# Kernel optimization log

Hardware: AMD Instinct MI355X
Metric: run time of the kernel (lower is better)

## Reference

```python
import jax, jax.numpy as jnp
import numpy as np

N = 16384      # number of nodes (pos rows)
S = 16384      # number of src nodes (src_pos rows)
E = 262144     # number of edges (COO entries)
D = 512        # embed_dim
H = 8          # num_heads
HD = D // H    # head_dim = 64
HID = 1024     # mlp hidden
MLP_IN = D + 3 * H  # 536
EPS = 1e-5


def layer_norm(x, g, b):
    mu = jnp.mean(x, axis=-1, keepdims=True)
    var = jnp.mean((x - mu) ** 2, axis=-1, keepdims=True)
    return (x - mu) * jax.lax.rsqrt(var + EPS) * g + b


def setup_inputs() -> dict:
    key = jax.random.key(0)
    ks = jax.random.split(key, 20)
    s = 1.0 / np.sqrt(D)
    sh = 1.0 / np.sqrt(HID)
    return {
        "x": jax.random.normal(ks[0], (N, D), jnp.float32),
        "Wq": jax.random.uniform(ks[1], (D, D), jnp.float32, -s, s),
        "bq": jnp.zeros((D,), jnp.float32),
        "Wk": jax.random.uniform(ks[2], (D, D), jnp.float32, -s, s),
        "bk": jnp.zeros((D,), jnp.float32),
        "g_att": jnp.ones((D,), jnp.float32),
        "b_att": jnp.zeros((D,), jnp.float32),
        "g_mlp": jnp.ones((D,), jnp.float32),
        "b_mlp": jnp.zeros((D,), jnp.float32),
        "W_in": jax.random.uniform(ks[3], (HID, MLP_IN), jnp.float32, -s, s),
        "b_in": jnp.zeros((HID,), jnp.float32),
        "W_out": jax.random.uniform(ks[4], (D, HID), jnp.float32, -sh, sh),
        "b_out": jnp.zeros((D,), jnp.float32),
        "att_bias": jax.random.normal(ks[5], (H, E), jnp.float32),
        "dist": jax.random.uniform(ks[6], (E,), jnp.float32, 0.5, 6.0),
        "pos": jax.random.normal(ks[7], (N, 3), jnp.float32),
        "src_pos": jax.random.normal(ks[8], (S, 3), jnp.float32),
        "row_index": jax.random.randint(ks[9], (E,), 0, N),
        "src_index": jax.random.randint(ks[10], (E,), 0, S),
        "org_to_src": jax.random.randint(ks[11], (S,), 0, N),
    }


def reference(x, Wq, bq, Wk, bk, g_att, b_att, g_mlp, b_mlp, W_in, b_in,
              W_out, b_out, att_bias, dist, pos, src_pos,
              row_index, src_index, org_to_src):
    n = x.shape[0]
    z = layer_norm(x, g_att, b_att)
    q = (z @ Wq.T + bq).reshape(n, H, HD)          # [N,H,hd]
    k = (z @ Wk.T + bk).reshape(n, H, HD)          # [N,H,hd]
    k_src = k[org_to_src]                          # [S,H,hd]
    # per-edge masked logits: q[row] . k_src[col] / sqrt(hd) + bias
    qe = q[row_index]                              # [E,H,hd]
    ke = k_src[src_index]                          # [E,H,hd]
    logits = jnp.einsum('ehd,ehd->eh', qe, ke) / jnp.sqrt(jnp.float32(HD))
    logits = logits + att_bias.T                   # [E,H]
    # segment (per-row) softmax over incident edges
    m = jax.ops.segment_max(logits, row_index, num_segments=n)
    p = jnp.exp(logits - m[row_index])
    den = jax.ops.segment_sum(p, row_index, num_segments=n)
    att = p / den[row_index]                       # [E,H]
    inv = jnp.where(dist == 0, 0.0, 1.0 / dist)[:, None]
    att = att * inv
    # sparse bmm: feat[h,row] += att * src_pos[col]; rowsum for centering
    sp = src_pos[src_index]                        # [E,3]
    feat = jax.ops.segment_sum(att[:, :, None] * sp[:, None, :],
                               row_index, num_segments=n)   # [N,H,3]
    rowsum = jax.ops.segment_sum(att, row_index, num_segments=n)  # [N,H]
    feat = feat - rowsum[:, :, None] * pos[:, None, :]
    feat = feat.reshape(n, H * 3)
    z2 = layer_norm(x, g_mlp, b_mlp)
    h = jax.nn.gelu(jnp.concatenate([z2, feat], axis=-1) @ W_in.T + b_in)
    return x + (h @ W_out.T + b_out)
```

## Files before the change

### kernel.cpp

```cpp
#include <hip/hip_runtime.h>
#include <math.h>


typedef unsigned short u16;
typedef __attribute__((ext_vector_type(8))) short bf16x8;
typedef __attribute__((ext_vector_type(4))) float f32x4;
typedef __attribute__((ext_vector_type(2))) float f32x2;

constexpr int N_NODES = 16384;
constexpr int E_EDGES = 262144;
constexpr int D = 512;
constexpr int KIN = 576;

constexpr size_t OFF_ZATT = 0;
constexpr size_t OFF_ZCAT = 16777216;
constexpr size_t OFF_WQK  = 35651584;
constexpr size_t OFF_BQK  = 36700160;
constexpr size_t OFF_WIN  = 36704256;
constexpr size_t OFF_WOUT = 37883904;
constexpr size_t OFF_QK   = 38932480;
constexpr size_t OFF_CNT  = 55709696;
constexpr size_t OFF_BKT  = 55775232;
constexpr size_t OFF_HBF  = 59969536;

static __device__ __forceinline__ u16 f2bf(float f) {
  union { float f; unsigned int u; } v; v.f = f;
  unsigned int u = v.u;
  u = u + 0x7FFFu + ((u >> 16) & 1u);
  return (u16)(u >> 16);
}
static __device__ __forceinline__ void gload16(const u16* g, u16* l) {
  __builtin_amdgcn_global_load_lds(
      (const __attribute__((address_space(1))) unsigned int*)g,
      (__attribute__((address_space(3))) unsigned int*)l, 16, 0, 0);
}

__global__ __launch_bounds__(256) void prep_weights(
    const float* __restrict__ Wq, const float* __restrict__ Wk,
    const float* __restrict__ bq, const float* __restrict__ bk,
    const float* __restrict__ W_in, const float* __restrict__ W_out,
    const int* __restrict__ row_index,
    u16* __restrict__ wqk, float* __restrict__ bqk,
    u16* __restrict__ win, u16* __restrict__ wout,
    int* __restrict__ cnt, int* __restrict__ bucket)
{
  const int gid = blockIdx.x * 256 + threadIdx.x;
  if (gid < 512 * 1024) {
    wqk[gid]  = f2bf(gid < 512 * 512 ? Wq[gid] : Wk[gid - 512 * 512]);
    wout[gid] = f2bf(W_out[gid]);
  }
  if (gid < 1024 * KIN) {
    const int r = gid / KIN, c = gid - r * KIN;
    win[gid] = f2bf(c < 536 ? W_in[r * 536 + c] : 0.f);
  }
  if (gid < 1024) bqk[gid] = gid < 512 ? bq[gid] : bk[gid - 512];
  if (gid < E_EDGES) {
    const int r = row_index[gid];
    const int p = atomicAdd(&cnt[r], 1);
    if (p < 64) bucket[(size_t)r * 64 + p] = gid;
  }
}

__global__ __launch_bounds__(256) void ln_kernel(
    const float* __restrict__ x,
    const float* __restrict__ g1, const float* __restrict__ b1,
    const float* __restrict__ g2, const float* __restrict__ b2,
    u16* __restrict__ zatt, u16* __restrict__ zcat)
{
  const int row = blockIdx.x;
  const int t = threadIdx.x;
  const float2 v = *(const float2*)(x + (size_t)row * D + t * 2);
  float s = v.x + v.y;
  float s2 = v.x * v.x + v.y * v.y;
#pragma unroll
  for (int m = 1; m < 64; m <<= 1) {
    s  += __shfl_xor(s, m, 64);
    s2 += __shfl_xor(s2, m, 64);
  }
  __shared__ float red[8];
  const int wv = t >> 6;
  if ((t & 63) == 0) { red[wv] = s; red[4 + wv] = s2; }
  __syncthreads();
  s  = red[0] + red[1] + red[2] + red[3];
  s2 = red[4] + red[5] + red[6] + red[7];
  const float mu = s * (1.f / D);
  const float var = s2 * (1.f / D) - mu * mu;
  const float rs = rsqrtf(var + 1e-5f);
  const int c0 = t * 2;
  const float n0 = (v.x - mu) * rs, n1 = (v.y - mu) * rs;
  zatt[(size_t)row * D + c0]       = f2bf(n0 * g1[c0] + b1[c0]);
  zatt[(size_t)row * D + c0 + 1]   = f2bf(n1 * g1[c0 + 1] + b1[c0 + 1]);
  zcat[(size_t)row * KIN + c0]     = f2bf(n0 * g2[c0] + b2[c0]);
  zcat[(size_t)row * KIN + c0 + 1] = f2bf(n1 * g2[c0 + 1] + b2[c0 + 1]);
  if (t < 64) zcat[(size_t)row * KIN + D + t] = 0;
}

template <int EPI, int WPE>
__global__ __launch_bounds__(256, WPE) void gemm_nt(
    const u16* __restrict__ A, const u16* __restrict__ B,
    const float* __restrict__ bias, const float* __restrict__ resid,
    void* __restrict__ Cout, int M, int Nn, int K)
{
  constexpr int BM = 128, BN = 128, BK = 32;
  __shared__ __align__(16) u16 As[2 * BM * BK];
  __shared__ __align__(16) u16 Bs[2 * BN * BK];
  const int tid = threadIdx.x;
  const int lane = tid & 63;
  const int wave = tid >> 6;
  const int m0 = blockIdx.x * BM;
  const int n0 = blockIdx.y * BN;
  const int wm = (wave >> 1) * 64;
  const int wn = (wave & 1) * 64;
  const int fr = lane & 15;
  const int fq = lane >> 4;
  const int srow = lane >> 2;
  const int skoff = (lane & 3) * 8;

  f32x4 acc[4][4];
#pragma unroll
  for (int i = 0; i < 4; ++i)
#pragma unroll
    for (int j = 0; j < 4; ++j) acc[i][j] = 0.f;

  for (int k0 = 0; k0 < K; k0 += 2 * BK) {
    __syncthreads();
#pragma unroll
    for (int t = 0; t < 2; ++t) {
#pragma unroll
      for (int r = 0; r < 2; ++r) {
        const int rowbase = r * 64 + wave * 16;
        gload16(A + (size_t)(m0 + rowbase + srow) * K + k0 + t * BK + skoff,
                As + t * (BM * BK) + rowbase * BK);
        gload16(B + (size_t)(n0 + rowbase + srow) * K + k0 + t * BK + skoff,
                Bs + t * (BN * BK) + rowbase * BK);
      }
    }
    __syncthreads();
#pragma unroll
    for (int t = 0; t < 2; ++t) {
      bf16x8 af[4], bfr[4];
#pragma unroll
      for (int mi = 0; mi < 4; ++mi)
        af[mi] = *(const bf16x8*)(As + t * (BM * BK) + (wm + mi * 16 + fr) * BK + fq * 8);
#pragma unroll
      for (int ni = 0; ni < 4; ++ni)
        bfr[ni] = *(const bf16x8*)(Bs + t * (BN * BK) + (wn + ni * 16 + fr) * BK + fq * 8);
#pragma unroll
      for (int mi = 0; mi < 4; ++mi)
#pragma unroll
        for (int ni = 0; ni < 4; ++ni)
          acc[mi][ni] = __builtin_amdgcn_mfma_f32_16x16x32_bf16(af[mi], bfr[ni], acc[mi][ni], 0, 0, 0);
    }
  }

#pragma unroll
  for (int mi = 0; mi < 4; ++mi) {
#pragma unroll
    for (int ni = 0; ni < 4; ++ni) {
      const int col = n0 + wn + ni * 16 + fr;
      const float bv = bias[col];
#pragma unroll
      for (int rr = 0; rr < 4; ++rr) {
        const int row = m0 + wm + mi * 16 + fq * 4 + rr;
        float v = acc[mi][ni][rr] + bv;
        if (EPI == 1) {
          const float nu = -1.5957691216057308f * (v + 0.044715f * v * v * v);
          const float sg = __builtin_amdgcn_rcpf(1.f + __expf(nu));
          ((u16*)Cout)[(size_t)row * Nn + col] = f2bf(v * sg);
        } else if (EPI == 2) {
          ((float*)Cout)[(size_t)row * Nn + col] = v + resid[(size_t)row * Nn + col];
        } else {
          const int pk = __builtin_amdgcn_cvt_pk_fp8_f32(v, v, 0, false);
          ((unsigned char*)Cout)[(size_t)row * Nn + col] = (unsigned char)(pk & 0xFF);
        }
      }
    }
  }
}

__global__ __launch_bounds__(256) void edge_csr(
    const unsigned char* __restrict__ qk8, const float* __restrict__ att_bias,
    const float* __restrict__ dist, const float* __restrict__ src_pos,
    const int* __restrict__ src_index, const int* __restrict__ org_to_src,
    const int* __restrict__ cnt, const int* __restrict__ bucket,
    const float* __restrict__ pos, u16* __restrict__ zcat)
{
  const int lane = threadIdx.x & 63;
  const int wave = threadIdx.x >> 6;
  const int row = blockIdx.x * 4 + wave;
  const int half = lane >> 5;
  const int sub = lane & 31;
  const int h = sub >> 2, j = sub & 3;
  const int deg = min(cnt[row], 64);
  const int base = row * 64;

  const uint4 qv = *(const uint4*)(qk8 + (size_t)row * 1024 + sub * 16);
  float qf[16];
  {
    const unsigned int* qu = (const unsigned int*)&qv;
#pragma unroll
    for (int i = 0; i < 4; ++i) {
      const f32x2 lo = __builtin_amdgcn_cvt_pk_f32_fp8(qu[i], false);
      const f32x2 hi = __builtin_amdgcn_cvt_pk_f32_fp8(qu[i], true);
      qf[i * 4 + 0] = lo.x; qf[i * 4 + 1] = lo.y;
      qf[i * 4 + 2] = hi.x; qf[i * 4 + 3] = hi.y;
    }
  }

  float accA = 0.f, accB = 0.f;
  const int npair = (deg + 1) >> 1;

  int idx = half;
  bool ok = idx < deg;
  int e = ok ? bucket[base + idx] : 0;
  int s = src_index[e];
  int kr = org_to_src[s];
  uint4 kv = *(const uint4*)(qk8 + (size_t)kr * 1024 + 512 + sub * 16);

  for (int i = 0; i < npair; ++i) {
    const int idx2 = idx + 2;
    const bool ok2 = idx2 < deg;
    const int e2 = ok2 ? bucket[base + idx2] : 0;
    const int s2 = src_index[e2];
    const int kr2 = org_to_src[s2];
    const uint4 kv2 = *(const uint4*)(qk8 + (size_t)kr2 * 1024 + 512 + sub * 16);

    const float bias_h = att_bias[(size_t)h * E_EDGES + e];
    const float dv = dist[e];
    const float spA = (j >= 2) ? src_pos[(size_t)s * 3 + (j - 2)] : 0.f;
    const float spB = (j == 1) ? src_pos[(size_t)s * 3 + 2] : 0.f;
    float p;
    {
      const unsigned int* ku = (const unsigned int*)&kv;
      const f32x2 a0 = __builtin_amdgcn_cvt_pk_f32_fp8(ku[0], false);
      const f32x2 a1 = __builtin_amdgcn_cvt_pk_f32_fp8(ku[0], true);
      const f32x2 b0 = __builtin_amdgcn_cvt_pk_f32_fp8(ku[1], false);
      const f32x2 b1 = __builtin_amdgcn_cvt_pk_f32_fp8(ku[1], true);
      const f32x2 c0 = __builtin_amdgcn_cvt_pk_f32_fp8(ku[2], false);
      const f32x2 c1 = __builtin_amdgcn_cvt_pk_f32_fp8(ku[2], true);
      const f32x2 d0 = __builtin_amdgcn_cvt_pk_f32_fp8(ku[3], false);
      const f32x2 d1 = __builtin_amdgcn_cvt_pk_f32_fp8(ku[3], true);
      p = qf[0] * a0.x;
      p = fmaf(qf[1],  a0.y, p);  p = fmaf(qf[2],  a1.x, p);  p = fmaf(qf[3],  a1.y, p);
      p = fmaf(qf[4],  b0.x, p);  p = fmaf(qf[5],  b0.y, p);  p = fmaf(qf[6],  b1.x, p);
      p = fmaf(qf[7],  b1.y, p);  p = fmaf(qf[8],  c0.x, p);  p = fmaf(qf[9],  c0.y, p);
      p = fmaf(qf[10], c1.x, p);  p = fmaf(qf[11], c1.y, p);  p = fmaf(qf[12], d0.x, p);
      p = fmaf(qf[13], d0.y, p);  p = fmaf(qf[14], d1.x, p);  p = fmaf(qf[15], d1.y, p);
    }
    p += __shfl_xor(p, 1, 64);
    p += __shfl_xor(p, 2, 64);
    float pe = __expf(p * 0.125f + bias_h);
    pe = ok ? pe : 0.f;
    const float w = (dv == 0.f) ? 0.f : pe / dv;
    accA += (j == 0) ? pe : (j == 1) ? w : w * spA;
    accB += w * spB;

    idx = idx2; ok = ok2; e = e2; s = s2; kv = kv2;
  }

  accA += __shfl_xor(accA, 32, 64);
  accB += __shfl_xor(accB, 32, 64);
  const int hb = h << 2;
  const float den  = __shfl(accA, hb + 0, 64);
  const float wsum = __shfl(accA, hb + 1, 64);
  const float wsp01 = __shfl(accA, hb + 2 + (j & 1), 64);
  const float wsp2  = __shfl(accB, hb + 1, 64);
  const float invd = (den != 0.f) ? 1.f / den : 0.f;
  const float rsum = wsum * invd;
  if (half == 0 && j < 3) {
    const float wspj = (j < 2) ? wsp01 : wsp2;
    zcat[(size_t)row * KIN + D + h * 3 + j] = f2bf(wspj * invd - rsum * pos[row * 3 + j]);
  }
}

extern "C" void kernel_launch(void* const* d_in, const int* in_sizes, int n_in,
                              void* d_out, int out_size, void* d_ws, size_t ws_size,
                              hipStream_t stream)
{
  const float* x        = (const float*)d_in[0];
  const float* Wq       = (const float*)d_in[1];
  const float* bq       = (const float*)d_in[2];
  const float* Wk       = (const float*)d_in[3];
  const float* bk       = (const float*)d_in[4];
  const float* g_att    = (const float*)d_in[5];
  const float* b_att    = (const float*)d_in[6];
  const float* g_mlp    = (const float*)d_in[7];
  const float* b_mlp    = (const float*)d_in[8];
  const float* W_in     = (const float*)d_in[9];
  const float* b_in     = (const float*)d_in[10];
  const float* W_out    = (const float*)d_in[11];
  const float* b_out    = (const float*)d_in[12];
  const float* att_bias = (const float*)d_in[13];
  const float* dist     = (const float*)d_in[14];
  const float* pos      = (const float*)d_in[15];
  const float* src_pos  = (const float*)d_in[16];
  const int* row_index  = (const int*)d_in[17];
  const int* src_index  = (const int*)d_in[18];
  const int* org_to_src = (const int*)d_in[19];

  char* ws = (char*)d_ws;
  u16*   zatt = (u16*)(ws + OFF_ZATT);
  u16*   zcat = (u16*)(ws + OFF_ZCAT);
  u16*   wqk  = (u16*)(ws + OFF_WQK);
  float* bqk  = (float*)(ws + OFF_BQK);
  u16*   win  = (u16*)(ws + OFF_WIN);
  u16*   wout = (u16*)(ws + OFF_WOUT);
  unsigned char* qk8 = (unsigned char*)(ws + OFF_QK);
  int*   cnt  = (int*)(ws + OFF_CNT);
  int*   bkt  = (int*)(ws + OFF_BKT);
  u16*   hbf  = (u16*)(ws + OFF_HBF);

  hipMemsetAsync(ws + OFF_CNT, 0, 65536, stream);

  prep_weights<<<2304, 256, 0, stream>>>(Wq, Wk, bq, bk, W_in, W_out, row_index,
                                         wqk, bqk, win, wout, cnt, bkt);
  ln_kernel<<<N_NODES, 256, 0, stream>>>(x, g_att, b_att, g_mlp, b_mlp, zatt, zcat);
  gemm_nt<4, 4><<<dim3(128, 8), 256, 0, stream>>>(zatt, wqk, bqk, nullptr, qk8, N_NODES, 1024, 512);
  edge_csr<<<N_NODES / 4, 256, 0, stream>>>(qk8, att_bias, dist, src_pos, src_index,
                                            org_to_src, cnt, bkt, pos, zcat);
  gemm_nt<1, 4><<<dim3(128, 8), 256, 0, stream>>>(zcat, win, b_in, nullptr, hbf, N_NODES, 1024, KIN);
  gemm_nt<2, 2><<<dim3(128, 4), 256, 0, stream>>>(hbf, wout, b_out, x, d_out, N_NODES, 512, 1024);
}
```

Baseline: 288.0 us.

## Pack per-edge attributes into contiguous records and deepen edge prefetch pipeline

The prep kernel now gathers each edge's eight attention biases, inverse distance, source position and key row index into one 64-byte record stored in the hidden-activation workspace, which is overwritten later. The edge kernel reads these records instead of doing several scattered dependent gathers (src_index, then org_to_src, strided att_bias, dist, src_pos). It also prefetches in three stages so the key row load has fewer dependent steps ahead of it. The cost is extra scattered writes and a random gather in the prep kernel, plus about 16 MB of new writes.

After: 268.0 us. 7.0% less time.

```diff
diff --git a/kernel.cpp b/kernel.cpp
--- a/kernel.cpp
+++ b/kernel.cpp
@@ -40,9 +40,12 @@
     const float* __restrict__ bq, const float* __restrict__ bk,
     const float* __restrict__ W_in, const float* __restrict__ W_out,
     const int* __restrict__ row_index,
+    const float* __restrict__ att_bias, const float* __restrict__ dist,
+    const float* __restrict__ src_pos, const int* __restrict__ src_index,
+    const int* __restrict__ org_to_src,
     u16* __restrict__ wqk, float* __restrict__ bqk,
     u16* __restrict__ win, u16* __restrict__ wout,
-    int* __restrict__ cnt, int* __restrict__ bucket)
+    int* __restrict__ cnt, int* __restrict__ bucket, float* __restrict__ rec)
 {
   const int gid = blockIdx.x * 256 + threadIdx.x;
   if (gid < 512 * 1024) {
@@ -58,6 +61,25 @@
     const int r = row_index[gid];
     const int p = atomicAdd(&cnt[r], 1);
     if (p < 64) bucket[(size_t)r * 64 + p] = gid;
+    const int s = src_index[gid];
+    const float dv = dist[gid];
+    float4 q0, q1, q2, q3;
+    q0.x = att_bias[gid];
+    q0.y = att_bias[(size_t)1 * E_EDGES + gid];
+    q0.z = att_bias[(size_t)2 * E_EDGES + gid];
+    q0.w = att_bias[(size_t)3 * E_EDGES + gid];
+    q1.x = att_bias[(size_t)4 * E_EDGES + gid];
+    q1.y = att_bias[(size_t)5 * E_EDGES + gid];
+    q1.z = att_bias[(size_t)6 * E_EDGES + gid];
+    q1.w = att_bias[(size_t)7 * E_EDGES + gid];
+    q2.x = (dv == 0.f) ? 0.f : 1.f / dv;
+    q2.y = src_pos[(size_t)s * 3 + 0];
+    q2.z = src_pos[(size_t)s * 3 + 1];
+    q2.w = src_pos[(size_t)s * 3 + 2];
+    q3.x = __int_as_float(org_to_src[s]);
+    q3.y = 0.f; q3.z = 0.f; q3.w = 0.f;
+    float4* rg = (float4*)(rec + (size_t)gid * 16);
+    rg[0] = q0; rg[1] = q1; rg[2] = q2; rg[3] = q3;
   }
 }
 
@@ -179,9 +201,7 @@
 }
 
 __global__ __launch_bounds__(256) void edge_csr(
-    const unsigned char* __restrict__ qk8, const float* __restrict__ att_bias,
-    const float* __restrict__ dist, const float* __restrict__ src_pos,
-    const int* __restrict__ src_index, const int* __restrict__ org_to_src,
+    const unsigned char* __restrict__ qk8, const float* __restrict__ rec,
     const int* __restrict__ cnt, const int* __restrict__ bucket,
     const float* __restrict__ pos, u16* __restrict__ zcat)
 {
@@ -210,28 +230,41 @@
   float accA = 0.f, accB = 0.f;
   const int npair = (deg + 1) >> 1;
 
-  int idx = half;
-  bool ok = idx < deg;
-  int e = ok ? bucket[base + idx] : 0;
-  int s = src_index[e];
-  int kr = org_to_src[s];
-  uint4 kv = *(const uint4*)(qk8 + (size_t)kr * 1024 + 512 + sub * 16);
+  bool ok0 = half < deg;
+  int e0 = ok0 ? bucket[base + half] : 0;
+  const float* r0 = rec + (size_t)e0 * 16;
+  float bias0 = r0[h];
+  float invd0 = r0[8];
+  float spA0 = (j >= 2) ? r0[7 + j] : 0.f;
+  float spB0 = (j == 1) ? r0[11] : 0.f;
+  uint4 kv0 = *(const uint4*)(qk8 + (size_t)__float_as_int(r0[12]) * 1024 + 512 + sub * 16);
+
+  bool ok1 = 2 + half < deg;
+  int e1 = ok1 ? bucket[base + 2 + half] : 0;
+  const float* r1 = rec + (size_t)e1 * 16;
+  float bias1 = r1[h];
+  float invd1 = r1[8];
+  float spA1 = (j >= 2) ? r1[7 + j] : 0.f;
+  float spB1 = (j == 1) ? r1[11] : 0.f;
+  int kr1 = __float_as_int(r1[12]);
+
+  bool ok2 = 4 + half < deg;
+  int e2 = ok2 ? bucket[base + 4 + half] : 0;
 
   for (int i = 0; i < npair; ++i) {
-    const int idx2 = idx + 2;
-    const bool ok2 = idx2 < deg;
-    const int e2 = ok2 ? bucket[base + idx2] : 0;
-    const int s2 = src_index[e2];
-    const int kr2 = org_to_src[s2];
-    const uint4 kv2 = *(const uint4*)(qk8 + (size_t)kr2 * 1024 + 512 + sub * 16);
-
-    const float bias_h = att_bias[(size_t)h * E_EDGES + e];
-    const float dv = dist[e];
-    const float spA = (j >= 2) ? src_pos[(size_t)s * 3 + (j - 2)] : 0.f;
-    const float spB = (j == 1) ? src_pos[(size_t)s * 3 + 2] : 0.f;
+    const uint4 kv1 = *(const uint4*)(qk8 + (size_t)kr1 * 1024 + 512 + sub * 16);
+    const float* r2 = rec + (size_t)e2 * 16;
+    const float bias2 = r2[h];
+    const float invd2 = r2[8];
+    const float spA2 = (j >= 2) ? r2[7 + j] : 0.f;
+    const float spB2 = (j == 1) ? r2[11] : 0.f;
+    const int kr2 = __float_as_int(r2[12]);
+    const bool ok3 = 2 * (i + 3) + half < deg;
+    const int e3 = ok3 ? bucket[base + 2 * (i + 3) + half] : 0;
+
     float p;
     {
-      const unsigned int* ku = (const unsigned int*)&kv;
+      const unsigned int* ku = (const unsigned int*)&kv0;
       const f32x2 a0 = __builtin_amdgcn_cvt_pk_f32_fp8(ku[0], false);
       const f32x2 a1 = __builtin_amdgcn_cvt_pk_f32_fp8(ku[0], true);
       const f32x2 b0 = __builtin_amdgcn_cvt_pk_f32_fp8(ku[1], false);
@@ -249,13 +282,15 @@
     }
     p += __shfl_xor(p, 1, 64);
     p += __shfl_xor(p, 2, 64);
-    float pe = __expf(p * 0.125f + bias_h);
-    pe = ok ? pe : 0.f;
-    const float w = (dv == 0.f) ? 0.f : pe / dv;
-    accA += (j == 0) ? pe : (j == 1) ? w : w * spA;
-    accB += w * spB;
-
-    idx = idx2; ok = ok2; e = e2; s = s2; kv = kv2;
+    float pe = __expf(p * 0.125f + bias0);
+    pe = ok0 ? pe : 0.f;
+    const float w = pe * invd0;
+    accA += (j == 0) ? pe : (j == 1) ? w : w * spA0;
+    accB += w * spB0;
+
+    ok0 = ok1; bias0 = bias1; invd0 = invd1; spA0 = spA1; spB0 = spB1; kv0 = kv1;
+    ok1 = ok2; bias1 = bias2; invd1 = invd2; spA1 = spA2; spB1 = spB2; kr1 = kr2;
+    ok2 = ok3; e2 = e3;
   }
 
   accA += __shfl_xor(accA, 32, 64);
@@ -309,15 +344,16 @@
   int*   cnt  = (int*)(ws + OFF_CNT);
   int*   bkt  = (int*)(ws + OFF_BKT);
   u16*   hbf  = (u16*)(ws + OFF_HBF);
+  float* rec  = (float*)(ws + OFF_HBF);
 
   hipMemsetAsync(ws + OFF_CNT, 0, 65536, stream);
 
   prep_weights<<<2304, 256, 0, stream>>>(Wq, Wk, bq, bk, W_in, W_out, row_index,
-                                         wqk, bqk, win, wout, cnt, bkt);
+                                         att_bias, dist, src_pos, src_index, org_to_src,
+                                         wqk, bqk, win, wout, cnt, bkt, rec);
   ln_kernel<<<N_NODES, 256, 0, stream>>>(x, g_att, b_att, g_mlp, b_mlp, zatt, zcat);
   gemm_nt<4, 4><<<dim3(128, 8), 256, 0, stream>>>(zatt, wqk, bqk, nullptr, qk8, N_NODES, 1024, 512);
-  edge_csr<<<N_NODES / 4, 256, 0, stream>>>(qk8, att_bias, dist, src_pos, src_index,
-                                            org_to_src, cnt, bkt, pos, zcat);
+  edge_csr<<<N_NODES / 4, 256, 0, stream>>>(qk8, rec, cnt, bkt, pos, zcat);
   gemm_nt<1, 4><<<dim3(128, 8), 256, 0, stream>>>(zcat, win, b_in, nullptr, hbf, N_NODES, 1024, KIN);
   gemm_nt<2, 2><<<dim3(128, 4), 256, 0, stream>>>(hbf, wout, b_out, x, d_out, N_NODES, 512, 1024);
 }
```
